# Performance work log

Measured on AMD Instinct MI355X. Metric: run time of the kernel, lower is better.

The kernel has to match this reference:

```python
import jax, jax.numpy as jnp
import numpy as np

EMBED = 512
HEADS = 1
HEAD_DIM = EMBED // HEADS  # 512 (heads must be 1 for the original torch code to run)
N, S = 4, 4096


def setup_inputs() -> dict:
    key = jax.random.key(0)
    ks = jax.random.split(key, 9)
    scale = 1.0 / np.sqrt(EMBED)
    return {
        "values": jax.random.normal(ks[0], (N, 1, S, EMBED), dtype=jnp.float32),
        "keys": jax.random.normal(ks[1], (N, 1, S, EMBED), dtype=jnp.float32),
        "query": jax.random.normal(ks[2], (N, 1, S, EMBED), dtype=jnp.float32),
        "mask": jax.random.randint(ks[3], (N, 1, S, S), 0, 2, dtype=jnp.int32),
        "Wv": jax.random.normal(ks[4], (EMBED, EMBED), dtype=jnp.float32) * scale,
        "Wk": jax.random.normal(ks[5], (EMBED, EMBED), dtype=jnp.float32) * scale,
        "Wq": jax.random.normal(ks[6], (EMBED, EMBED), dtype=jnp.float32) * scale,
        "Wo": jax.random.normal(ks[7], (EMBED, EMBED), dtype=jnp.float32) * scale,
        "bo": jnp.zeros((EMBED,), dtype=jnp.float32),
    }


def reference(values, keys, query, mask, Wv, Wk, Wq, Wo, bo):
    n = query.shape[0]
    q_len = query.shape[2]
    # reshape(N, -1, heads, head_dim); inputs are [N, 1, S, E] -> [N, S, H, Dh]
    v = values.reshape(n, -1, HEADS, HEAD_DIM)
    k = keys.reshape(n, -1, HEADS, HEAD_DIM)
    q = query.reshape(n, -1, HEADS, HEAD_DIM)
    # per-module linear projections (nn.Linear: y = x @ W.T)
    v = jnp.einsum('nlhd,ed->nlhe', v, Wv)
    k = jnp.einsum('nlhd,ed->nlhe', k, Wk)
    q = jnp.einsum('nqhd,ed->nqhe', q, Wq)
    # full [N, H, Q, K] score matrix, as in the original
    energy = jnp.einsum('nqhd,nkhd->nhqk', q, k)
    energy = jnp.where(mask == 0, jnp.float32(-1e20), energy)
    attn = jax.nn.softmax(energy / np.sqrt(HEAD_DIM), axis=3)
    out = jnp.einsum('nhql,nlhd->nqhd', attn, v).reshape(n, q_len, HEADS * HEAD_DIM)
    return out @ Wo.T + bo
```

## Files before the change

kernel.cpp:

```cpp
#include <hip/hip_runtime.h>

typedef __bf16 bf16x8 __attribute__((ext_vector_type(8)));
typedef __bf16 bf16x4 __attribute__((ext_vector_type(4)));
typedef float f32x4 __attribute__((ext_vector_type(4)));
typedef float f32x16 __attribute__((ext_vector_type(16)));

#define MFMA16(a, b, c) __builtin_amdgcn_mfma_f32_16x16x32_bf16((a), (b), (c), 0, 0, 0)
#define MFMA32(a, b, c) __builtin_amdgcn_mfma_f32_32x32x16_bf16((a), (b), (c), 0, 0, 0)

static constexpr int SEQ = 4096;
static constexpr int DIM = 512;

typedef __attribute__((address_space(3))) void lds_void;
typedef __attribute__((address_space(1))) const void gbl_void;

__device__ __forceinline__ void glds16(const void* g, void* l) {
    __builtin_amdgcn_global_load_lds((gbl_void*)g, (lds_void*)l, 16, 0, 0);
}

__device__ __forceinline__ bf16x8 cvt8f(const float* __restrict__ p) {
    float4 f0 = *(const float4*)p;
    float4 f1 = *(const float4*)(p + 4);
    bf16x8 v;
    v[0] = (__bf16)f0.x; v[1] = (__bf16)f0.y; v[2] = (__bf16)f0.z; v[3] = (__bf16)f0.w;
    v[4] = (__bf16)f1.x; v[5] = (__bf16)f1.y; v[6] = (__bf16)f1.z; v[7] = (__bf16)f1.w;
    return v;
}

__global__ __launch_bounds__(256)
void convert_w(const float* __restrict__ wq, const float* __restrict__ wk,
               const float* __restrict__ wv, const float* __restrict__ wo,
               __bf16* __restrict__ out)
{
    const int z = blockIdx.y;
    const float* src = (z == 0) ? wq : (z == 1) ? wk : (z == 2) ? wv : wo;
    __bf16* dst = out + (size_t)z * DIM * DIM;
    const int i = (blockIdx.x * 256 + threadIdx.x) * 8;
    *(bf16x8*)(dst + i) = cvt8f(src + i);
}

__global__ __launch_bounds__(256, 3)
void gemm_qkv(const float* __restrict__ Aq, const float* __restrict__ Ak,
              const float* __restrict__ Av, const __bf16* __restrict__ Wb,
              __bf16* __restrict__ Qp, __bf16* __restrict__ Kp,
              __bf16* __restrict__ Vtp)
{
    const int z = blockIdx.z;
    const float* Ap = (z == 0) ? Aq : (z == 1) ? Ak : Av;
    const __bf16* Bp = Wb + (size_t)z * DIM * DIM;
    __bf16* Cp = (z == 0) ? Qp : (z == 1) ? Kp : Vtp;

    __shared__ __align__(16) char smem[128 * 132 * 2];
    __bf16* As = (__bf16*)smem;
    __bf16* Bs = (__bf16*)(smem + 16384);

    const int tid  = threadIdx.x;
    const int wave = tid >> 6;
    const int lane = tid & 63;
    const int quad = lane >> 4;
    const int l16  = lane & 15;
    const int m0 = blockIdx.x * 128;
    const int n0 = blockIdx.y * 128;
    const int wm = (wave >> 1) * 64;
    const int wn = (wave & 1) * 64;

    f32x4 acc[4][4] = {};

    for (int k0 = 0; k0 < DIM; k0 += 64) {
        #pragma unroll
        for (int i = 0; i < 4; i++) {
            const int j = wave * 4 + i;
            const int t = j * 64 + lane;
            const int row = t >> 3, c8 = t & 7;
            glds16(Bp + (size_t)(n0 + row) * DIM + k0 + c8 * 8, &Bs[j * 512]);
            *(bf16x8*)&As[t * 8] =
                cvt8f(Ap + (size_t)(m0 + row) * DIM + k0 + c8 * 8);
        }
        __syncthreads();
        #pragma unroll
        for (int kk = 0; kk < 2; kk++) {
            bf16x8 af[4], bg[4];
            #pragma unroll
            for (int mt = 0; mt < 4; mt++)
                af[mt] = *(const bf16x8*)&As[(wm + mt * 16 + l16) * 64 + kk * 32 + quad * 8];
            #pragma unroll
            for (int nt = 0; nt < 4; nt++)
                bg[nt] = *(const bf16x8*)&Bs[(wn + nt * 16 + l16) * 64 + kk * 32 + quad * 8];
            #pragma unroll
            for (int mt = 0; mt < 4; mt++)
                #pragma unroll
                for (int nt = 0; nt < 4; nt++)
                    acc[mt][nt] = MFMA16(af[mt], bg[nt], acc[mt][nt]);
        }
        __syncthreads();
    }

    if (z < 2) {
        #pragma unroll
        for (int mt = 0; mt < 4; mt++)
            #pragma unroll
            for (int nt = 0; nt < 4; nt++)
                #pragma unroll
                for (int r = 0; r < 4; r++)
                    Cp[(size_t)(m0 + wm + mt * 16 + quad * 4 + r) * DIM
                       + n0 + wn + nt * 16 + l16] = (__bf16)acc[mt][nt][r];
    } else {
        __bf16* Tt = (__bf16*)smem;
        __syncthreads();
        #pragma unroll
        for (int mt = 0; mt < 4; mt++)
            #pragma unroll
            for (int nt = 0; nt < 4; nt++)
                #pragma unroll
                for (int r = 0; r < 4; r++)
                    Tt[(wm + mt * 16 + quad * 4 + r) * 132 + wn + nt * 16 + l16]
                        = (__bf16)acc[mt][nt][r];
        __syncthreads();
        const int nb  = m0 >> 12;
        const int s0m = m0 & 4095;
        const int d   = tid >> 1;
        const int sh  = (tid & 1) * 64;
        __bf16* dst = Cp + (size_t)nb * DIM * SEQ + (size_t)(n0 + d) * SEQ + s0m + sh;
        #pragma unroll
        for (int i = 0; i < 8; i++) {
            bf16x8 vv;
            #pragma unroll
            for (int e = 0; e < 8; e++) vv[e] = Tt[(sh + i * 8 + e) * 132 + d];
            *(bf16x8*)(dst + i * 8) = vv;
        }
    }
}

__global__ __launch_bounds__(256, 3)
void gemm_out(const __bf16* __restrict__ Ap, const __bf16* __restrict__ Bp,
              float* __restrict__ Cp, const float* __restrict__ bias)
{
    __shared__ __align__(16) __bf16 As[128 * 64];
    __shared__ __align__(16) __bf16 Bs[128 * 64];
    const int tid  = threadIdx.x;
    const int wave = tid >> 6;
    const int lane = tid & 63;
    const int quad = lane >> 4;
    const int l16  = lane & 15;
    const int m0 = blockIdx.x * 128;
    const int n0 = blockIdx.y * 128;
    const int wm = (wave >> 1) * 64;
    const int wn = (wave & 1) * 64;

    f32x4 acc[4][4] = {};

    for (int k0 = 0; k0 < DIM; k0 += 64) {
        #pragma unroll
        for (int i = 0; i < 4; i++) {
            const int j = wave * 4 + i;
            const int c = j * 64 + lane;
            const int row = c >> 3, c8 = c & 7;
            glds16(Ap + (size_t)(m0 + row) * DIM + k0 + c8 * 8, &As[j * 512]);
            glds16(Bp + (size_t)(n0 + row) * DIM + k0 + c8 * 8, &Bs[j * 512]);
        }
        __syncthreads();
        #pragma unroll
        for (int kk = 0; kk < 2; kk++) {
            bf16x8 af[4], bg[4];
            #pragma unroll
            for (int mt = 0; mt < 4; mt++)
                af[mt] = *(const bf16x8*)&As[(wm + mt * 16 + l16) * 64 + kk * 32 + quad * 8];
            #pragma unroll
            for (int nt = 0; nt < 4; nt++)
                bg[nt] = *(const bf16x8*)&Bs[(wn + nt * 16 + l16) * 64 + kk * 32 + quad * 8];
            #pragma unroll
            for (int mt = 0; mt < 4; mt++)
                #pragma unroll
                for (int nt = 0; nt < 4; nt++)
                    acc[mt][nt] = MFMA16(af[mt], bg[nt], acc[mt][nt]);
        }
        __syncthreads();
    }
    #pragma unroll
    for (int mt = 0; mt < 4; mt++)
        #pragma unroll
        for (int nt = 0; nt < 4; nt++)
            #pragma unroll
            for (int r = 0; r < 4; r++) {
                const int col = n0 + wn + nt * 16 + l16;
                Cp[(size_t)(m0 + wm + mt * 16 + quad * 4 + r) * DIM + col]
                    = acc[mt][nt][r] + bias[col];
            }
}

#define MKC(v, r4) ((r4) == 0 ? (v).x : (r4) == 1 ? (v).y : (r4) == 2 ? (v).z : (v).w)
#define WAITLGKM() asm volatile("s_waitcnt lgkmcnt(0)" ::: "memory")
#define BARRIER()  asm volatile("s_barrier" ::: "memory")

__global__ __launch_bounds__(512, 1)
void flash_attn(__bf16* __restrict__ Qp, const __bf16* __restrict__ Kp,
                const __bf16* __restrict__ Vt, const int* __restrict__ mask)
{
    constexpr float SCALE = 0.044194173824159216f;
    constexpr int QPITCH = 520;

    __shared__ __bf16 Qs[64 * QPITCH];
    __shared__ __bf16 P[64 * 256];
    __shared__ float pmax[8 * 66];
    __shared__ float psum[8 * 66];

    const int bid  = blockIdx.x;
    const int n    = bid & 3;
    const int q0   = (bid >> 2) * 64;
    const int tid  = threadIdx.x;
    const int w    = tid >> 6;
    const int lane = tid & 63;
    const int l32  = lane & 31;
    const int half = lane >> 5;

    const __bf16* Qb = Qp + (size_t)n * SEQ * DIM;
    const __bf16* Kb = Kp + (size_t)n * SEQ * DIM;
    const __bf16* Vb = Vt + (size_t)n * DIM * SEQ;
    const int*    Mb = mask + (size_t)n * SEQ * SEQ;
    __bf16*       AO = Qp + (size_t)n * SEQ * DIM;

    #pragma unroll
    for (int i = 0; i < 8; i++) {
        const int r  = i * 8 + w;
        const int hr = (r & 7) ^ ((r >> 3) & 7);
        const int cs = (lane & 56) | ((lane & 7) ^ hr);
        glds16(Qb + (size_t)(q0 + r) * DIM + cs * 8, &Qs[r * QPITCH]);
    }

    const __bf16* kPtr  = Kb + (size_t)(32 * w + l32) * DIM + half * 8;
    const __bf16* vPtr0 = Vb + (size_t)(32 * w + l32) * SEQ + half * 8;
    const __bf16* vPtr1 = vPtr0 + (size_t)256 * SEQ;

    const int h0 = (l32 & 7) ^ ((l32 >> 3) & 7);
    const int h1 = h0 ^ 4;
    int q0off[4], q1off[4];
    #pragma unroll
    for (int ks = 0; ks < 4; ks++) {
        q0off[ks] = ((2 * ks + half) ^ h0) * 8;
        q1off[ks] = ((2 * ks + half) ^ h1) * 8;
    }
    const int qrow0 = l32 * QPITCH;
    const int qrow1 = (32 + l32) * QPITCH;

    float m0 = -__builtin_inff(), m1 = -__builtin_inff();
    float l0 = 0.f, l1 = 0.f;
    f32x16 o00 = {}, o01 = {}, o10 = {}, o11 = {};
    f32x16 s0, s1;

    bf16x8 kA[4], kB[4], vA[4], vB[4];

#define LOADK(buf, dc_) { _Pragma("unroll") \
    for (int ks = 0; ks < 4; ks++) \
        buf[ks] = *(const bf16x8*)(kPtr + (dc_) * 64 + ks * 16); }

#define LOADV(buf, vc_) { const __bf16* vp_ = ((vc_) < 4) ? vPtr0 : vPtr1; \
    _Pragma("unroll") \
    for (int ks = 0; ks < 4; ks++) \
        buf[ks] = *(const bf16x8*)(vp_ + ((vc_) & 3) * 64 + ks * 16); }

#define QK8(buf, dc_) { __builtin_amdgcn_s_setprio(1); \
    _Pragma("unroll") \
    for (int ks = 0; ks < 4; ks++) { \
        bf16x8 b0 = *(const bf16x8*)&Qs[qrow0 + (dc_) * 64 + q0off[ks]]; \
        bf16x8 b1 = *(const bf16x8*)&Qs[qrow1 + (dc_) * 64 + q1off[ks]]; \
        s0 = MFMA32(buf[ks], b0, s0); \
        s1 = MFMA32(buf[ks], b1, s1); \
    } __builtin_amdgcn_s_setprio(0); }

#define PV8(buf, vc_) { __builtin_amdgcn_s_setprio(1); \
    _Pragma("unroll") \
    for (int ks = 0; ks < 4; ks++) { \
        const int ck = ((vc_) & 3) * 8 + 2 * ks + half; \
        const int cp = (ck & 24) | ((ck & 7) ^ (l32 & 7)); \
        bf16x8 b0 = *(const bf16x8*)&P[l32 * 256 + cp * 8]; \
        bf16x8 b1 = *(const bf16x8*)&P[(32 + l32) * 256 + cp * 8]; \
        if ((vc_) < 4) { o00 = MFMA32(buf[ks], b0, o00); o01 = MFMA32(buf[ks], b1, o01); } \
        else           { o10 = MFMA32(buf[ks], b0, o10); o11 = MFMA32(buf[ks], b1, o11); } \
    } __builtin_amdgcn_s_setprio(0); }

    __syncthreads();
    LOADK(kA, 0);

    #pragma unroll 1
    for (int j = 0; j < 16; j++) {
        const int k0 = j * 256;

        int4 mk0[4], mk1[4];
        {
            const int* mp0 = Mb + (size_t)(q0 + l32) * SEQ + k0 + 32 * w + 4 * half;
            const int* mp1 = mp0 + (size_t)32 * SEQ;
            #pragma unroll
            for (int g = 0; g < 4; g++) {
                mk0[g] = *(const int4*)(mp0 + 8 * g);
                mk1[g] = *(const int4*)(mp1 + 8 * g);
            }
        }

        s0 = (f32x16){}; s1 = (f32x16){};
        LOADK(kB, 1); QK8(kA, 0);
        LOADK(kA, 2); QK8(kB, 1);
        LOADK(kB, 3); QK8(kA, 2);
        LOADK(kA, 4); QK8(kB, 3);
        LOADK(kB, 5); QK8(kA, 4);
        LOADK(kA, 6); QK8(kB, 5);
        LOADK(kB, 7); QK8(kA, 6);
                      QK8(kB, 7);

        {
            float mx0 = s0[0], mx1 = s1[0];
            #pragma unroll
            for (int r = 1; r < 16; r++) { mx0 = fmaxf(mx0, s0[r]); mx1 = fmaxf(mx1, s1[r]); }
            mx0 = fmaxf(mx0, __shfl_xor(mx0, 32));
            mx1 = fmaxf(mx1, __shfl_xor(mx1, 32));
            if (half == 0) pmax[w * 66 + l32]      = mx0;
            else           pmax[w * 66 + 32 + l32] = mx1;
        }
        WAITLGKM();
        BARRIER();

        LOADV(vA, 0);

        float mp0v = pmax[l32], mp1v = pmax[32 + l32];
        #pragma unroll
        for (int w2 = 1; w2 < 8; w2++) {
            mp0v = fmaxf(mp0v, pmax[w2 * 66 + l32]);
            mp1v = fmaxf(mp1v, pmax[w2 * 66 + 32 + l32]);
        }
        const float mn0 = fmaxf(m0, mp0v * SCALE);
        const float mn1 = fmaxf(m1, mp1v * SCALE);
        const float a0 = __expf(m0 - mn0);
        const float a1 = __expf(m1 - mn1);
        m0 = mn0; m1 = mn1;
        #pragma unroll
        for (int r = 0; r < 16; r++) {
            o00[r] *= a0; o10[r] *= a0;
            o01[r] *= a1; o11[r] *= a1;
        }

        float ls0 = 0.f, ls1 = 0.f;
        #pragma unroll
        for (int g = 0; g < 4; g++) {
            bf16x4 pv0, pv1;
            #pragma unroll
            for (int r4 = 0; r4 < 4; r4++) {
                const int r = g * 4 + r4;
                float p0 = __expf(s0[r] * SCALE - mn0);
                float p1 = __expf(s1[r] * SCALE - mn1);
                p0 = MKC(mk0[g], r4) ? p0 : 0.f;
                p1 = MKC(mk1[g], r4) ? p1 : 0.f;
                ls0 += p0; ls1 += p1;
                pv0[r4] = (__bf16)p0;
                pv1[r4] = (__bf16)p1;
            }
            const int c  = 4 * w + g;
            const int cp = (c & 24) | ((c & 7) ^ (l32 & 7));
            *(bf16x4*)&P[l32 * 256 + cp * 8 + 4 * half]        = pv0;
            *(bf16x4*)&P[(32 + l32) * 256 + cp * 8 + 4 * half] = pv1;
        }
        ls0 += __shfl_xor(ls0, 32);
        ls1 += __shfl_xor(ls1, 32);
        if (half == 0) psum[w * 66 + l32]      = ls0;
        else           psum[w * 66 + 32 + l32] = ls1;
        WAITLGKM();
        BARRIER();

        {
            float ss0 = 0.f, ss1 = 0.f;
            #pragma unroll
            for (int w2 = 0; w2 < 8; w2++) {
                ss0 += psum[w2 * 66 + l32];
                ss1 += psum[w2 * 66 + 32 + l32];
            }
            l0 = l0 * a0 + ss0;
            l1 = l1 * a1 + ss1;
        }

        LOADV(vB, 1); PV8(vA, 0);
        LOADV(vA, 2); PV8(vB, 1);
        LOADV(vB, 3); PV8(vA, 2);
        LOADV(vA, 4); PV8(vB, 3);
        LOADV(vB, 5); PV8(vA, 4);
        LOADV(vA, 6); PV8(vB, 5);
        LOADV(vB, 7); PV8(vA, 6);
                      PV8(vB, 7);

        kPtr  += 256 * DIM;
        vPtr0 += 256;
        vPtr1 += 256;
        if (j < 15) LOADK(kA, 0);
        WAITLGKM();
        BARRIER();
    }

    const float li0 = 1.f / l0, li1 = 1.f / l1;
    __bf16* ao0 = AO + (size_t)(q0 + l32) * DIM;
    __bf16* ao1 = AO + (size_t)(q0 + 32 + l32) * DIM;
    #pragma unroll
    for (int h = 0; h < 2; h++) {
        #pragma unroll
        for (int g = 0; g < 4; g++) {
            bf16x4 v00, v01;
            #pragma unroll
            for (int r4 = 0; r4 < 4; r4++) {
                const int r = g * 4 + r4;
                v00[r4] = (__bf16)((h ? o10[r] : o00[r]) * li0);
                v01[r4] = (__bf16)((h ? o11[r] : o01[r]) * li1);
            }
            const int d = h * 256 + 32 * w + g * 8 + 4 * half;
            *(bf16x4*)&ao0[d] = v00;
            *(bf16x4*)&ao1[d] = v01;
        }
    }
#undef LOADK
#undef LOADV
#undef QK8
#undef PV8
}

extern "C" void kernel_launch(void* const* d_in, const int* in_sizes, int n_in,
                              void* d_out, int out_size, void* d_ws, size_t ws_size,
                              hipStream_t stream)
{
    const float* values = (const float*)d_in[0];
    const float* keys   = (const float*)d_in[1];
    const float* query  = (const float*)d_in[2];
    const int*   mask   = (const int*)d_in[3];
    const float* Wv = (const float*)d_in[4];
    const float* Wk = (const float*)d_in[5];
    const float* Wq = (const float*)d_in[6];
    const float* Wo = (const float*)d_in[7];
    const float* bo = (const float*)d_in[8];
    float* out = (float*)d_out;

    char* ws = (char*)d_ws;
    __bf16* Qp  = (__bf16*)(ws);
    __bf16* Kp  = (__bf16*)(ws + (16u << 20));
    __bf16* Vt  = (__bf16*)(ws + (32u << 20));
    __bf16* wbf = (__bf16*)(ws + (48u << 20));

    const int M = 4 * SEQ;

    convert_w<<<dim3(128, 4), 256, 0, stream>>>(Wq, Wk, Wv, Wo, wbf);

    gemm_qkv<<<dim3(M / 128, DIM / 128, 3), 256, 0, stream>>>(
        query, keys, values, wbf, Qp, Kp, Vt);

    flash_attn<<<256, 512, 0, stream>>>(Qp, Kp, Vt, mask);

    gemm_out<<<dim3(M / 128, DIM / 128), 256, 0, stream>>>(
        Qp , wbf + 3 * DIM * DIM, out, bo);
}
```

Baseline: 728.1 us.

## Triple-buffer K/V register prefetch and replace LDS XOR swizzle with padded pitch

Register prefetch of K and V tiles goes from double to triple buffering, so global loads run two chunks ahead of the MFMA work. The first V chunks are issued during the QK phase and the next iteration's K chunks during the PV phase. The XOR swizzle on the Q and P shared-memory tiles is removed; P now uses a padded row pitch and Q a plain layout, which simplifies address math. The extra buffers raise VGPR pressure, and dropping the swizzle on Q may bring back LDS bank conflicts.

```diff
diff --git a/kernel.cpp b/kernel.cpp
--- a/kernel.cpp
+++ b/kernel.cpp
@@ -198,9 +198,10 @@
 {
     constexpr float SCALE = 0.044194173824159216f;
     constexpr int QPITCH = 520;
-
-    __shared__ __bf16 Qs[64 * QPITCH];
-    __shared__ __bf16 P[64 * 256];
+    constexpr int PPITCH = 264;
+
+    __shared__ __align__(16) __bf16 Qs[64 * QPITCH];
+    __shared__ __align__(16) __bf16 P[64 * PPITCH];
     __shared__ float pmax[8 * 66];
     __shared__ float psum[8 * 66];
 
@@ -221,24 +222,14 @@
 
     #pragma unroll
     for (int i = 0; i < 8; i++) {
-        const int r  = i * 8 + w;
-        const int hr = (r & 7) ^ ((r >> 3) & 7);
-        const int cs = (lane & 56) | ((lane & 7) ^ hr);
-        glds16(Qb + (size_t)(q0 + r) * DIM + cs * 8, &Qs[r * QPITCH]);
+        const int r = i * 8 + w;
+        glds16(Qb + (size_t)(q0 + r) * DIM + lane * 8, &Qs[r * QPITCH]);
     }
 
     const __bf16* kPtr  = Kb + (size_t)(32 * w + l32) * DIM + half * 8;
     const __bf16* vPtr0 = Vb + (size_t)(32 * w + l32) * SEQ + half * 8;
     const __bf16* vPtr1 = vPtr0 + (size_t)256 * SEQ;
 
-    const int h0 = (l32 & 7) ^ ((l32 >> 3) & 7);
-    const int h1 = h0 ^ 4;
-    int q0off[4], q1off[4];
-    #pragma unroll
-    for (int ks = 0; ks < 4; ks++) {
-        q0off[ks] = ((2 * ks + half) ^ h0) * 8;
-        q1off[ks] = ((2 * ks + half) ^ h1) * 8;
-    }
     const int qrow0 = l32 * QPITCH;
     const int qrow1 = (32 + l32) * QPITCH;
 
@@ -247,11 +238,11 @@
     f32x16 o00 = {}, o01 = {}, o10 = {}, o11 = {};
     f32x16 s0, s1;
 
-    bf16x8 kA[4], kB[4], vA[4], vB[4];
-
-#define LOADK(buf, dc_) { _Pragma("unroll") \
+    bf16x8 kA[4], kB[4], kC[4], vA[4], vB[4], vC[4];
+
+#define LOADKB(buf, base, dc_) { _Pragma("unroll") \
     for (int ks = 0; ks < 4; ks++) \
-        buf[ks] = *(const bf16x8*)(kPtr + (dc_) * 64 + ks * 16); }
+        buf[ks] = *(const bf16x8*)((base) + (dc_) * 64 + ks * 16); }
 
 #define LOADV(buf, vc_) { const __bf16* vp_ = ((vc_) < 4) ? vPtr0 : vPtr1; \
     _Pragma("unroll") \
@@ -261,8 +252,8 @@
 #define QK8(buf, dc_) { __builtin_amdgcn_s_setprio(1); \
     _Pragma("unroll") \
     for (int ks = 0; ks < 4; ks++) { \
-        bf16x8 b0 = *(const bf16x8*)&Qs[qrow0 + (dc_) * 64 + q0off[ks]]; \
-        bf16x8 b1 = *(const bf16x8*)&Qs[qrow1 + (dc_) * 64 + q1off[ks]]; \
+        bf16x8 b0 = *(const bf16x8*)&Qs[qrow0 + (dc_) * 64 + (2 * ks + half) * 8]; \
+        bf16x8 b1 = *(const bf16x8*)&Qs[qrow1 + (dc_) * 64 + (2 * ks + half) * 8]; \
         s0 = MFMA32(buf[ks], b0, s0); \
         s1 = MFMA32(buf[ks], b1, s1); \
     } __builtin_amdgcn_s_setprio(0); }
@@ -271,15 +262,15 @@
     _Pragma("unroll") \
     for (int ks = 0; ks < 4; ks++) { \
         const int ck = ((vc_) & 3) * 8 + 2 * ks + half; \
-        const int cp = (ck & 24) | ((ck & 7) ^ (l32 & 7)); \
-        bf16x8 b0 = *(const bf16x8*)&P[l32 * 256 + cp * 8]; \
-        bf16x8 b1 = *(const bf16x8*)&P[(32 + l32) * 256 + cp * 8]; \
+        bf16x8 b0 = *(const bf16x8*)&P[l32 * PPITCH + ck * 8]; \
+        bf16x8 b1 = *(const bf16x8*)&P[(32 + l32) * PPITCH + ck * 8]; \
         if ((vc_) < 4) { o00 = MFMA32(buf[ks], b0, o00); o01 = MFMA32(buf[ks], b1, o01); } \
         else           { o10 = MFMA32(buf[ks], b0, o10); o11 = MFMA32(buf[ks], b1, o11); } \
     } __builtin_amdgcn_s_setprio(0); }
 
     __syncthreads();
-    LOADK(kA, 0);
+    LOADKB(kA, kPtr, 0);
+    LOADKB(kB, kPtr, 1);
 
     #pragma unroll 1
     for (int j = 0; j < 16; j++) {
@@ -297,14 +288,15 @@
         }
 
         s0 = (f32x16){}; s1 = (f32x16){};
-        LOADK(kB, 1); QK8(kA, 0);
-        LOADK(kA, 2); QK8(kB, 1);
-        LOADK(kB, 3); QK8(kA, 2);
-        LOADK(kA, 4); QK8(kB, 3);
-        LOADK(kB, 5); QK8(kA, 4);
-        LOADK(kA, 6); QK8(kB, 5);
-        LOADK(kB, 7); QK8(kA, 6);
-                      QK8(kB, 7);
+        LOADKB(kC, kPtr, 2);
+        QK8(kA, 0); LOADKB(kA, kPtr, 3);
+        QK8(kB, 1); LOADKB(kB, kPtr, 4);
+        QK8(kC, 2); LOADKB(kC, kPtr, 5);
+        QK8(kA, 3); LOADKB(kA, kPtr, 6);
+        QK8(kB, 4); LOADKB(kB, kPtr, 7);
+        QK8(kC, 5); LOADV(vA, 0);
+        QK8(kA, 6); LOADV(vB, 1);
+        QK8(kB, 7); LOADV(vC, 2);
 
         {
             float mx0 = s0[0], mx1 = s1[0];
@@ -317,8 +309,6 @@
         }
         WAITLGKM();
         BARRIER();
-
-        LOADV(vA, 0);
 
         float mp0v = pmax[l32], mp1v = pmax[32 + l32];
         #pragma unroll
@@ -352,10 +342,9 @@
                 pv0[r4] = (__bf16)p0;
                 pv1[r4] = (__bf16)p1;
             }
-            const int c  = 4 * w + g;
-            const int cp = (c & 24) | ((c & 7) ^ (l32 & 7));
-            *(bf16x4*)&P[l32 * 256 + cp * 8 + 4 * half]        = pv0;
-            *(bf16x4*)&P[(32 + l32) * 256 + cp * 8 + 4 * half] = pv1;
+            const int c = 4 * w + g;
+            *(bf16x4*)&P[l32 * PPITCH + c * 8 + 4 * half]        = pv0;
+            *(bf16x4*)&P[(32 + l32) * PPITCH + c * 8 + 4 * half] = pv1;
         }
         ls0 += __shfl_xor(ls0, 32);
         ls1 += __shfl_xor(ls1, 32);
@@ -375,19 +364,18 @@
             l1 = l1 * a1 + ss1;
         }
 
-        LOADV(vB, 1); PV8(vA, 0);
-        LOADV(vA, 2); PV8(vB, 1);
-        LOADV(vB, 3); PV8(vA, 2);
-        LOADV(vA, 4); PV8(vB, 3);
-        LOADV(vB, 5); PV8(vA, 4);
-        LOADV(vA, 6); PV8(vB, 5);
-        LOADV(vB, 7); PV8(vA, 6);
-                      PV8(vB, 7);
+        PV8(vA, 0); LOADV(vA, 3);
+        PV8(vB, 1); LOADV(vB, 4);
+        PV8(vC, 2); LOADV(vC, 5);
+        PV8(vA, 3); LOADV(vA, 6);
+        PV8(vB, 4); LOADV(vB, 7);
+        PV8(vC, 5); if (j < 15) LOADKB(kA, kPtr + 256 * DIM, 0);
+        PV8(vA, 6); if (j < 15) LOADKB(kB, kPtr + 256 * DIM, 1);
+        PV8(vB, 7);
 
         kPtr  += 256 * DIM;
         vPtr0 += 256;
         vPtr1 += 256;
-        if (j < 15) LOADK(kA, 0);
         WAITLGKM();
         BARRIER();
     }
@@ -411,7 +399,7 @@
             *(bf16x4*)&ao1[d] = v01;
         }
     }
-#undef LOADK
+#undef LOADKB
 #undef LOADV
 #undef QK8
 #undef PV8
```

Result: no change. 724.2 us (-0.5%).
